# Performance work log

Hardware: AMD Instinct MI355X
Metric: run time of the kernel (lower is better)

The kernel has to match this reference:

```python
import jax, jax.numpy as jnp
import numpy as np

H = 150
PASSES = 5
NSETS = 2
N = 50000
E = 400000
G = 64
SLOPE = 0.01  # torch leaky_relu default


def setup_inputs() -> dict:
    key = jax.random.key(0)
    ks = jax.random.split(key, 20)
    def u(k, shape, fan):
        lim = 1.0 / np.sqrt(fan)
        return jax.random.uniform(k, shape, jnp.float32, -lim, lim)
    return {
        "nodes": jax.random.normal(ks[0], (N, H), jnp.float32),
        "problem_type": jax.random.uniform(ks[1], (G, 1), jnp.float32),
        "edge_W": u(ks[2], (NSETS, H, H), H),
        "edge_b": u(ks[3], (NSETS, H), H),
        "gru_w_ih": u(ks[4], (3 * H, H), H),
        "gru_w_hh": u(ks[5], (3 * H, H), H),
        "gru_b_ih": u(ks[6], (3 * H,), H),
        "gru_b_hh": u(ks[7], (3 * H,), H),
        "fc1_w": u(ks[8], (80, 151), 151),
        "fc1_b": u(ks[9], (80,), 151),
        "fc2_w": u(ks[10], (80, 80), 80),
        "fc2_b": u(ks[11], (80,), 80),
        "fcL_w": u(ks[12], (10, 80), 80),
        "fcL_b": u(ks[13], (10,), 80),
        "edges": jax.random.randint(ks[14], (NSETS, E, 2), 0, N),
        "graph_ids": jnp.sort(jax.random.randint(ks[15], (N,), 0, G)),
        "tbptt": 0,
    }


def _gru_cell(x, h, w_ih, w_hh, b_ih, b_hh):
    gi = x @ w_ih.T + b_ih  # [N, 3H]
    gh = h @ w_hh.T + b_hh
    ir, iz, inn = jnp.split(gi, 3, axis=-1)
    hr, hz, hn = jnp.split(gh, 3, axis=-1)
    r = jax.nn.sigmoid(ir + hr)
    z = jax.nn.sigmoid(iz + hz)
    n = jnp.tanh(inn + r * hn)
    return (1.0 - z) * n + z * h


def reference(nodes, problem_type, edge_W, edge_b, gru_w_ih, gru_w_hh,
              gru_b_ih, gru_b_hh, fc1_w, fc1_b, fc2_w, fc2_b, fcL_w, fcL_b,
              edges, graph_ids, tbptt):
    n_sets = edge_W.shape[0]
    n_graphs = problem_type.shape[0]
    for j in range(PASSES):
        incoming = jnp.zeros_like(nodes)
        for k in range(n_sets):
            src = edges[k, :, 1]
            dst = edges[k, :, 0]
            # NOTE: in the source, the first Linear+leaky_relu result is
            # overwritten; the effective edge message is just the second Linear.
            y = nodes[src] @ edge_W[k].T + edge_b[k]  # [E, H]
            incoming = incoming.at[dst].add(y)
        nodes = _gru_cell(incoming, nodes, gru_w_ih, gru_w_hh, gru_b_ih, gru_b_hh)
        if tbptt == 1 and j < PASSES - 2:
            nodes = jax.lax.stop_gradient(nodes)
    g = jax.ops.segment_sum(nodes, graph_ids, num_segments=n_graphs)  # [G, H]
    g = jnp.log(g)
    g = jnp.where(jnp.isnan(g), 0.0, g)
    g = jax.nn.relu(g)
    x = jnp.concatenate([g, problem_type], axis=1)  # [G, 151]
    x = jax.nn.leaky_relu(x @ fc1_w.T + fc1_b, SLOPE)
    x = jax.nn.leaky_relu(x @ fc2_w.T + fc2_b, SLOPE)
    return x @ fcL_w.T + fcL_b  # [G, 10]
```

## Files before the change

kernel.cpp:

```cpp
#include <hip/hip_runtime.h>
#include <stdint.h>

#define NN 50000
#define H 150
#define NE 400000
#define NG 64
#define NPASS 5
#define KB 480
#define VC 640
#define NRB 391

typedef unsigned short u16;
typedef unsigned int u32;
typedef __attribute__((ext_vector_type(8))) short short8;
typedef __attribute__((ext_vector_type(4))) float float4v;
typedef __attribute__((ext_vector_type(4))) u32 uint4v;

__device__ __forceinline__ u16 f2bf_rn(float x) {
  union { float f; u32 u; } v; v.f = x;
  u32 r = v.u + 0x7fffu + ((v.u >> 16) & 1u);
  return (u16)(r >> 16);
}
__device__ __forceinline__ float bf2f(u16 h) {
  union { u32 u; float f; } v; v.u = ((u32)h) << 16;
  return v.f;
}
__device__ __forceinline__ u32 packf(float v) {
  u16 hi = f2bf_rn(v);
  u16 lo = f2bf_rn(v - bf2f(hi));
  return (u32)hi | ((u32)lo << 16);
}
__device__ __forceinline__ float upk(u32 u) {
  union { u32 u; float f; } a, b;
  a.u = u << 16; b.u = u & 0xffff0000u;
  return a.f + b.f;
}
__device__ __forceinline__ void async16(const void* g, void* l) {
  __builtin_amdgcn_global_load_lds(
      (const __attribute__((address_space(1))) unsigned int*)(uintptr_t)g,
      (__attribute__((address_space(3))) unsigned int*)(uint32_t)(uintptr_t)l,
      16, 0, 0);
}

__global__ void hist_kernel(const int* __restrict__ edges, int* __restrict__ cnt) {
  int id = blockIdx.x * 256 + threadIdx.x;
  if (id >= 2 * NE) return;
  int dst = edges[id * 2];
  int set = id / NE;
  atomicAdd(&cnt[dst * 2 + set], 1);
}

__global__ __launch_bounds__(1024) void scan1_kernel(const int* __restrict__ cnt,
                                                     int* __restrict__ rowptr,
                                                     int* __restrict__ bsum, int n) {
  __shared__ int sd[1024];
  int t = threadIdx.x;
  int idx = blockIdx.x * 1024 + t;
  int v = (idx < n) ? cnt[idx] : 0;
  sd[t] = v;
  __syncthreads();
  for (int off = 1; off < 1024; off <<= 1) {
    int add = (t >= off) ? sd[t - off] : 0;
    __syncthreads();
    sd[t] += add;
    __syncthreads();
  }
  if (idx < n) rowptr[idx] = sd[t] - v;
  if (t == 1023) bsum[blockIdx.x] = sd[1023];
}

__global__ __launch_bounds__(128) void scan2_kernel(const int* __restrict__ bsum,
                                                    int* __restrict__ boff, int nb) {
  __shared__ int sd[128];
  int t = threadIdx.x;
  int v = (t < nb) ? bsum[t] : 0;
  sd[t] = v;
  __syncthreads();
  for (int off = 1; off < 128; off <<= 1) {
    int add = (t >= off) ? sd[t - off] : 0;
    __syncthreads();
    sd[t] += add;
    __syncthreads();
  }
  boff[t] = sd[t] - v;
}

__global__ void scan3_kernel(int* __restrict__ rowptr, const int* __restrict__ boff, int n) {
  int idx = blockIdx.x * 256 + threadIdx.x;
  if (idx < n) rowptr[idx] += boff[idx >> 10];
}

__global__ void total_kernel(int* __restrict__ rowptr, const int* __restrict__ boff, int n, int nb) {
  if (threadIdx.x == 0 && blockIdx.x == 0) rowptr[n] = boff[nb];
}

__global__ void copy_int_kernel(const int* __restrict__ a, int* __restrict__ b, int n) {
  int id = blockIdx.x * 256 + threadIdx.x;
  if (id < n) b[id] = a[id];
}

__global__ void fill_kernel(const int* __restrict__ edges, int* __restrict__ cursor,
                            u16* __restrict__ colbuf) {
  int id = blockIdx.x * 256 + threadIdx.x;
  if (id >= 2 * NE) return;
  int dst = edges[id * 2];
  int src = edges[id * 2 + 1];
  int set = id / NE;
  int pos = atomicAdd(&cursor[dst * 2 + set], 1);
  colbuf[pos] = (u16)src;
}

__global__ void bounds_kernel(const int* __restrict__ gids, int* __restrict__ gstart) {
  int g = threadIdx.x;
  if (g > NG) return;
  int lo = 0, hi = NN;
  while (lo < hi) { int m = (lo + hi) >> 1; if (gids[m] < g) lo = m + 1; else hi = m; }
  gstart[g] = lo;
}

__global__ void build_B_kernel(const float* __restrict__ wih, const float* __restrict__ whh,
                               const float* __restrict__ eW,
                               u16* __restrict__ Bh, u16* __restrict__ Bl) {
  int id = blockIdx.x * 256 + threadIdx.x;
  if (id >= VC * KB) return;
  int v = id / KB, k = id % KB;
  int g = (v >> 4) & 3, c = (v >> 6) * 16 + (v & 15);
  int seg = k / 160, kk = k % 160;
  float val = 0.f;
  if (c < H && kk < H) {
    if (seg < 2) {
      if (g < 3) {
        const float* wr = wih + (size_t)(g * H + c) * H;
        const float* wc = eW + (size_t)seg * H * H + kk;
        float acc = 0.f;
        for (int t = 0; t < H; t++) acc += wr[t] * wc[(size_t)t * H];
        val = acc;
      }
    } else {
      if (g == 0) val = whh[(size_t)c * H + kk];
      else if (g == 1) val = whh[(size_t)(H + c) * H + kk];
      else if (g == 3) val = whh[(size_t)(2 * H + c) * H + kk];
    }
  }
  u16 h = f2bf_rn(val);
  Bh[id] = h;
  Bl[id] = f2bf_rn(val - bf2f(h));
}

__global__ void build_coef_kernel(const float* __restrict__ wih,
                                  const float* __restrict__ eb,
                                  const float* __restrict__ bih, const float* __restrict__ bhh,
                                  float* __restrict__ coefs) {
  int id = threadIdx.x + blockIdx.x * 256;
  if (id >= VC) return;
  int g = id / 160, c = id % 160;
  float u0 = 0.f, u1 = 0.f, bs = 0.f;
  if (c < H) {
    if (g < 3) {
      const float* wr = wih + (size_t)(g * H + c) * H;
      for (int t = 0; t < H; t++) { u0 += wr[t] * eb[t]; u1 += wr[t] * eb[H + t]; }
    }
    if (g == 0) bs = bih[c] + bhh[c];
    else if (g == 1) bs = bih[H + c] + bhh[H + c];
    else if (g == 2) bs = bih[2 * H + c];
    else bs = bhh[2 * H + c];
  }
  coefs[id] = u0;
  coefs[VC + id] = u1;
  coefs[2 * VC + id] = bs;
}

__global__ void init_nodes_kernel(const float* __restrict__ nin,
                                  u32* __restrict__ npkA, u32* __restrict__ npkB) {
  int id = blockIdx.x * 256 + threadIdx.x;
  if (id >= NN * 160) return;
  int r = id / 160, c = id % 160;
  if (c < H) {
    npkA[id] = packf(nin[(size_t)r * H + c]);
  } else {
    npkA[id] = 0;
    npkB[id] = 0;
  }
}

__global__ void pad_S_kernel(u32* __restrict__ Snp) {
  int id = blockIdx.x * 256 + threadIdx.x;
  if (id >= NN * 20) return;
  int r = id / 20, rem = id % 20;
  int set = rem / 10, t = rem % 10;
  Snp[(size_t)r * 320 + set * 160 + H + t] = 0;
}

__global__ __launch_bounds__(256) void gather_kernel(
    const u32* __restrict__ npk, const int* __restrict__ rowptr,
    const u16* __restrict__ colbuf, u32* __restrict__ Snp) {
  int gtid = blockIdx.x * 256 + threadIdx.x;
  int wid = gtid >> 6;
  if (wid >= 2 * NN) return;
  int node = wid >> 1, set = wid & 1;
  int lane = gtid & 63;
  int s = rowptr[2 * node + set], e = rowptr[2 * node + set + 1];
  int deg = e - s;
  int c4 = 4 * lane;
  bool ok = (lane < 40);
  float a0 = 0.f, a1 = 0.f, a2 = 0.f, a3 = 0.f;
  for (int base = 0; base < deg; base += 64) {
    int rem = min(64, deg - base);
    u32 srcv = 0;
    if (lane < rem) srcv = (u32)colbuf[s + base + lane];
    int i = 0;
    for (; i + 3 < rem; i += 4) {
      int r0 = __builtin_amdgcn_readlane((int)srcv, i);
      int r1 = __builtin_amdgcn_readlane((int)srcv, i + 1);
      int r2 = __builtin_amdgcn_readlane((int)srcv, i + 2);
      int r3 = __builtin_amdgcn_readlane((int)srcv, i + 3);
      uint4v v0 = {0, 0, 0, 0}, v1 = {0, 0, 0, 0};
      uint4v v2 = {0, 0, 0, 0}, v3 = {0, 0, 0, 0};
      if (ok) {
        v0 = *(const uint4v*)(npk + (size_t)(u32)r0 * 160 + c4);
        v1 = *(const uint4v*)(npk + (size_t)(u32)r1 * 160 + c4);
        v2 = *(const uint4v*)(npk + (size_t)(u32)r2 * 160 + c4);
        v3 = *(const uint4v*)(npk + (size_t)(u32)r3 * 160 + c4);
      }
      a0 += upk(v0.x) + upk(v1.x);
      a1 += upk(v0.y) + upk(v1.y);
      a2 += upk(v0.z) + upk(v1.z);
      a3 += upk(v0.w) + upk(v1.w);
      a0 += upk(v2.x) + upk(v3.x);
      a1 += upk(v2.y) + upk(v3.y);
      a2 += upk(v2.z) + upk(v3.z);
      a3 += upk(v2.w) + upk(v3.w);
    }
    for (; i + 1 < rem; i += 2) {
      int r0 = __builtin_amdgcn_readlane((int)srcv, i);
      int r1 = __builtin_amdgcn_readlane((int)srcv, i + 1);
      uint4v v0 = {0, 0, 0, 0}, v1 = {0, 0, 0, 0};
      if (ok) {
        v0 = *(const uint4v*)(npk + (size_t)(u32)r0 * 160 + c4);
        v1 = *(const uint4v*)(npk + (size_t)(u32)r1 * 160 + c4);
      }
      a0 += upk(v0.x) + upk(v1.x);
      a1 += upk(v0.y) + upk(v1.y);
      a2 += upk(v0.z) + upk(v1.z);
      a3 += upk(v0.w) + upk(v1.w);
    }
    if (i < rem) {
      int r0 = __builtin_amdgcn_readlane((int)srcv, i);
      uint4v v0 = {0, 0, 0, 0};
      if (ok) v0 = *(const uint4v*)(npk + (size_t)(u32)r0 * 160 + c4);
      a0 += upk(v0.x);
      a1 += upk(v0.y);
      a2 += upk(v0.z);
      a3 += upk(v0.w);
    }
  }
  if (ok) {
    uint4v pv;
    pv.x = packf(a0);
    pv.y = packf(a1);
    pv.z = packf(a2);
    pv.w = packf(a3);
    *(uint4v*)(Snp + (size_t)node * 320 + set * 160 + c4) = pv;
  }
}


template<int KT>
__device__ __forceinline__ void stage_fn(
    const u32* __restrict__ Snp, const u32* __restrict__ npkc,
    const u16* __restrict__ Bhp, const u16* __restrict__ Blp,
    char* Ab, char* Bb, int tid, int w, int r0, int ccb) {
  #pragma unroll
  for (int i = 0; i < 4; i++) {
    int cl = i * 256 + tid;
    int row = cl >> 3;
    int q = (cl & 7) ^ (row & 7);
    int rg = min(r0 + row, NN - 1);
    if constexpr (KT < 10)
      async16(Snp + (size_t)rg * 320 + KT * 32 + q * 4, Ab + i * 4096 + w * 1024);
    else
      async16(npkc + (size_t)rg * 160 + (KT - 10) * 32 + q * 4, Ab + i * 4096 + w * 1024);
  }
  constexpr int koffB = (KT < 10) ? KT * 32 : 320 + (KT - 10) * 32;
  constexpr int skipg = (KT < 10) ? 3 : 2;
  #pragma unroll
  for (int i = 0; i < 2; i++) {
    int cl = i * 256 + tid;
    int row = cl >> 2;
    int q = (cl & 3) ^ ((row >> 1) & 3);
    if (((row >> 4) & 3) != skipg) {
      size_t gb = (size_t)(ccb * 128 + row) * KB + koffB + q * 8;
      int lb = i * 4096 + w * 1024;
      async16(Bhp + gb, Bb + lb);
      async16(Blp + gb, Bb + 8192 + lb);
    }
  }
}

template<int KTn>
__device__ __forceinline__ void read_frags_fn(
    const char* Ab, const char* Bb, int m, int quad, int mrow0, int nco0,
    uint4v (&A0)[4], uint4v (&A1)[4], short8 (&RBh)[3], short8 (&RBl)[3]) {
  #pragma unroll
  for (int jj = 0; jj < 3; jj++) {
    const int jsel = (jj == 2) ? ((KTn < 10) ? 2 : 3) : jj;
    int br = nco0 + jsel * 16 + m;
    int bd = br * 64 + ((quad ^ ((br >> 1) & 3)) * 16);
    RBh[jj] = *(const short8*)(Bb + bd);
    RBl[jj] = *(const short8*)(Bb + 8192 + bd);
  }
  #pragma unroll
  for (int mt = 0; mt < 4; mt++) {
    int r = mrow0 + mt * 16 + m;
    A0[mt] = *(const uint4v*)(Ab + r * 128 + (((2 * quad) ^ (r & 7)) * 16));
    A1[mt] = *(const uint4v*)(Ab + r * 128 + (((2 * quad + 1) ^ (r & 7)) * 16));
  }
}

template<int KT>
__device__ __forceinline__ void mfma_fn(
    const uint4v (&A0)[4], const uint4v (&A1)[4],
    const short8 (&MBh)[3], const short8 (&MBl)[3], float4v (&acc)[4][4]) {
  #pragma unroll
  for (int mt = 0; mt < 4; mt++) {
    u32 uu[8] = {A0[mt].x, A0[mt].y, A0[mt].z, A0[mt].w,
                 A1[mt].x, A1[mt].y, A1[mt].z, A1[mt].w};
    short8 ah, al;
    #pragma unroll
    for (int e2 = 0; e2 < 8; e2++) {
      ah[e2] = (short)(uu[e2] & 0xffffu);
      al[e2] = (short)(uu[e2] >> 16);
    }
    #pragma unroll
    for (int jj = 0; jj < 3; jj++) {
      const int J = (KT < 10) ? jj : ((jj == 2) ? 3 : jj);
      acc[mt][J] = __builtin_amdgcn_mfma_f32_16x16x32_bf16(ah, MBh[jj], acc[mt][J], 0, 0, 0);
      acc[mt][J] = __builtin_amdgcn_mfma_f32_16x16x32_bf16(ah, MBl[jj], acc[mt][J], 0, 0, 0);
      acc[mt][J] = __builtin_amdgcn_mfma_f32_16x16x32_bf16(al, MBh[jj], acc[mt][J], 0, 0, 0);
    }
  }
}

template<int KT>
__device__ __forceinline__ void gemm_step(
    const u32* __restrict__ Snp, const u32* __restrict__ npkc,
    const u16* __restrict__ Bhp, const u16* __restrict__ Blp,
    char (&Abuf)[16384], char (&Bbuf)[16384],
    int tid, int w, int m, int quad, int mrow0, int nco0, int r0, int ccb,
    float4v (&acc)[4][4]) {
  uint4v A0[4], A1[4];
  short8 FBh[3], FBl[3];
  read_frags_fn<KT>(Abuf, Bbuf, m, quad, mrow0, nco0, A0, A1, FBh, FBl);
  asm volatile("s_waitcnt lgkmcnt(0)" ::: "memory");
  __builtin_amdgcn_sched_barrier(0);
  __builtin_amdgcn_s_barrier();
  if constexpr (KT + 1 <= 14)
    stage_fn<KT + 1>(Snp, npkc, Bhp, Blp, Abuf, Bbuf, tid, w, r0, ccb);
  __builtin_amdgcn_sched_barrier(0);
  __builtin_amdgcn_s_setprio(1);
  mfma_fn<KT>(A0, A1, FBh, FBl, acc);
  __builtin_amdgcn_s_setprio(0);
  __builtin_amdgcn_sched_barrier(0);
  if constexpr (KT + 1 <= 14) {
    asm volatile("s_waitcnt vmcnt(0)" ::: "memory");
    __builtin_amdgcn_sched_barrier(0);
    __builtin_amdgcn_s_barrier();
  }
}

__global__ __launch_bounds__(256, 4) void gru_gemm_kernel(
    const u32* __restrict__ Snp, const u32* __restrict__ npkc,
    const u16* __restrict__ Bhp, const u16* __restrict__ Blp,
    const float* __restrict__ coefs, const int* __restrict__ rowptr,
    u32* __restrict__ npkn) {
  __shared__ char Abuf[16384];
  __shared__ char Bbuf[16384];
  const int bid = blockIdx.x;
  const int xcd = bid & 7;
  const int rest = bid >> 3;
  const int ccb = rest % 5;
  const int r0b = (rest / 5) * 8 + xcd;
  if (r0b >= NRB) return;
  const int r0 = r0b * 128;
  const int tid = threadIdx.x;
  const int w = tid >> 6, l = tid & 63;
  const int m = l & 15, quad = l >> 4;
  const int mrow0 = (w & 1) * 64;
  const int nco0 = (w >> 1) * 64;

  float4v acc[4][4];
  #pragma unroll
  for (int mt = 0; mt < 4; mt++)
    #pragma unroll
    for (int j = 0; j < 4; j++) acc[mt][j] = (float4v){0.f, 0.f, 0.f, 0.f};

  stage_fn<0>(Snp, npkc, Bhp, Blp, Abuf, Bbuf, tid, w, r0, ccb);
  asm volatile("s_waitcnt vmcnt(0)" ::: "memory");
  __builtin_amdgcn_sched_barrier(0);
  __builtin_amdgcn_s_barrier();

  #define STEP(K) gemm_step<K>(Snp, npkc, Bhp, Blp, Abuf, Bbuf, tid, w, m, quad, \
                               mrow0, nco0, r0, ccb, acc)
  STEP(0);  STEP(1);  STEP(2);  STEP(3);  STEP(4);
  STEP(5);  STEP(6);  STEP(7);  STEP(8);  STEP(9);
  STEP(10); STEP(11); STEP(12); STEP(13); STEP(14);
  #undef STEP

  int c = (ccb * 2 + (w >> 1)) * 16 + m;
  if (c >= H) return;
  float u0r = coefs[c],            u0z = coefs[160 + c],
        u0n = coefs[320 + c];
  float u1r = coefs[VC + c],       u1z = coefs[VC + 160 + c],
        u1n = coefs[VC + 320 + c];
  float bsr = coefs[2 * VC + c],   bsz = coefs[2 * VC + 160 + c],
        bsn = coefs[2 * VC + 320 + c], bsh = coefs[2 * VC + 480 + c];
  #pragma unroll
  for (int mt = 0; mt < 4; mt++) {
    #pragma unroll
    for (int i = 0; i < 4; i++) {
      int row = r0 + mrow0 + mt * 16 + quad * 4 + i;
      if (row >= NN) continue;
      float d0 = (float)(rowptr[2 * row + 1] - rowptr[2 * row]);
      float d1 = (float)(rowptr[2 * row + 2] - rowptr[2 * row + 1]);
      float pr = acc[mt][0][i] + d0 * u0r + d1 * u1r + bsr;
      float pz = acc[mt][1][i] + d0 * u0z + d1 * u1z + bsz;
      float pn = acc[mt][2][i] + d0 * u0n + d1 * u1n + bsn;
      float ph = acc[mt][3][i] + bsh;
      float r_g = 1.f / (1.f + __expf(-pr));
      float z_g = 1.f / (1.f + __expf(-pz));
      float narg = pn + r_g * ph;
      float e2 = __expf(2.f * narg);
      float n_g = 1.f - 2.f / (e2 + 1.f);
      float h = upk(npkc[(size_t)row * 160 + c]);
      npkn[(size_t)row * 160 + c] = packf((1.f - z_g) * n_g + z_g * h);
    }
  }
}

__global__ __launch_bounds__(192) void segsum_kernel(const u32* __restrict__ npk,
                                                     const int* __restrict__ gstart,
                                                     float* __restrict__ gsum) {
  int g = blockIdx.x, chunk = blockIdx.y;
  int c = threadIdx.x;
  if (c >= H) return;
  int s = gstart[g], e = gstart[g + 1];
  int len = e - s;
  if (len <= 0) return;
  int per = (len + 3) / 4;
  int rs = s + chunk * per;
  int re = min(e, rs + per);
  if (rs >= re) return;
  float acc = 0.f;
  for (int r = rs; r < re; r++) acc += upk(npk[(size_t)r * 160 + c]);
  atomicAdd(&gsum[g * H + c], acc);
}

__global__ __launch_bounds__(192) void head_kernel(
    const float* __restrict__ gsum, const float* __restrict__ pt,
    const float* __restrict__ fc1_w, const float* __restrict__ fc1_b,
    const float* __restrict__ fc2_w, const float* __restrict__ fc2_b,
    const float* __restrict__ fcL_w, const float* __restrict__ fcL_b,
    float* __restrict__ out) {
  __shared__ float x[151];
  __shared__ float x1[80];
  __shared__ float x2[80];
  int row = blockIdx.x;
  int t = threadIdx.x;
  if (t < 151) {
    float v;
    if (t < H) { float g = gsum[row * H + t]; v = (g > 1.f) ? logf(g) : 0.f; }
    else v = pt[row];
    x[t] = v;
  }
  __syncthreads();
  if (t < 80) {
    float acc = fc1_b[t];
    const float* wrow = fc1_w + t * 151;
    #pragma unroll 4
    for (int k = 0; k < 151; k++) acc += x[k] * wrow[k];
    x1[t] = (acc > 0.f) ? acc : 0.01f * acc;
  }
  __syncthreads();
  if (t < 80) {
    float acc = fc2_b[t];
    const float* wrow = fc2_w + t * 80;
    #pragma unroll 4
    for (int k = 0; k < 80; k++) acc += x1[k] * wrow[k];
    x2[t] = (acc > 0.f) ? acc : 0.01f * acc;
  }
  __syncthreads();
  if (t < 10) {
    float acc = fcL_b[t];
    const float* wrow = fcL_w + t * 80;
    #pragma unroll 4
    for (int k = 0; k < 80; k++) acc += x2[k] * wrow[k];
    out[row * 10 + t] = acc;
  }
}

extern "C" void kernel_launch(void* const* d_in, const int* in_sizes, int n_in,
                              void* d_out, int out_size, void* d_ws, size_t ws_size,
                              hipStream_t stream) {
  const float* nodes_in = (const float*)d_in[0];
  const float* problem_type = (const float*)d_in[1];
  const float* edge_W = (const float*)d_in[2];
  const float* edge_b = (const float*)d_in[3];
  const float* w_ih = (const float*)d_in[4];
  const float* w_hh = (const float*)d_in[5];
  const float* b_ih = (const float*)d_in[6];
  const float* b_hh = (const float*)d_in[7];
  const float* fc1_w = (const float*)d_in[8];
  const float* fc1_b = (const float*)d_in[9];
  const float* fc2_w = (const float*)d_in[10];
  const float* fc2_b = (const float*)d_in[11];
  const float* fcL_w = (const float*)d_in[12];
  const float* fcL_b = (const float*)d_in[13];
  const int* edges = (const int*)d_in[14];
  const int* graph_ids = (const int*)d_in[15];

  char* ws = (char*)d_ws;
  size_t off = 0;
  auto alloc = [&](size_t bytes) -> void* {
    void* p = ws + off;
    off = (off + bytes + 255) & ~(size_t)255;
    return p;
  };
  u32* npkA     = (u32*)alloc((size_t)NN * 160 * 4);
  u32* npkB     = (u32*)alloc((size_t)NN * 160 * 4);
  u32* Snp      = (u32*)alloc((size_t)NN * 320 * 4);
  u16* Bh       = (u16*)alloc((size_t)VC * KB * 2);
  u16* Bl       = (u16*)alloc((size_t)VC * KB * 2);
  float* coefs  = (float*)alloc(3 * VC * 4);
  int* rowptr   = (int*)alloc((2 * NN + 1) * 4);
  int* cursor   = (int*)alloc(2 * NN * 4);
  u16* colbuf   = (u16*)alloc(2ull * NE * 2);
  int* bsum     = (int*)alloc(128 * 4);
  int* boff     = (int*)alloc(128 * 4);
  int* gstart   = (int*)alloc((NG + 1) * 4);
  float* gsum   = (float*)alloc((size_t)NG * H * 4);

  const int n2 = 2 * NN;
  const int nb = (n2 + 1023) / 1024;

  hipMemsetAsync(cursor, 0, n2 * 4, stream);
  hist_kernel<<<(2 * NE + 255) / 256, 256, 0, stream>>>(edges, cursor);
  scan1_kernel<<<nb, 1024, 0, stream>>>(cursor, rowptr, bsum, n2);
  scan2_kernel<<<1, 128, 0, stream>>>(bsum, boff, nb);
  scan3_kernel<<<(n2 + 255) / 256, 256, 0, stream>>>(rowptr, boff, n2);
  total_kernel<<<1, 64, 0, stream>>>(rowptr, boff, n2, nb);
  copy_int_kernel<<<(n2 + 255) / 256, 256, 0, stream>>>(rowptr, cursor, n2);
  fill_kernel<<<(2 * NE + 255) / 256, 256, 0, stream>>>(edges, cursor, colbuf);
  bounds_kernel<<<1, 128, 0, stream>>>(graph_ids, gstart);
  build_B_kernel<<<(VC * KB + 255) / 256, 256, 0, stream>>>(w_ih, w_hh, edge_W, Bh, Bl);
  build_coef_kernel<<<(VC + 255) / 256, 256, 0, stream>>>(w_ih, edge_b, b_ih, b_hh, coefs);
  init_nodes_kernel<<<(NN * 160 + 255) / 256, 256, 0, stream>>>(nodes_in, npkA, npkB);
  pad_S_kernel<<<(NN * 20 + 255) / 256, 256, 0, stream>>>(Snp);

  const int ngrp = (NRB + 7) / 8;
  u32* nbuf[2] = {npkA, npkB};
  for (int pass = 0; pass < NPASS; pass++) {
    u32* cur = nbuf[pass & 1];
    u32* nxt = nbuf[1 - (pass & 1)];
    gather_kernel<<<(2 * NN * 64 + 255) / 256, 256, 0, stream>>>(cur, rowptr, colbuf, Snp);
    gru_gemm_kernel<<<ngrp * 5 * 8, 256, 0, stream>>>(
        Snp, cur, Bh, Bl, coefs, rowptr, nxt);
  }
  u32* fin = nbuf[NPASS & 1];

  hipMemsetAsync(gsum, 0, (size_t)NG * H * 4, stream);
  segsum_kernel<<<dim3(NG, 4), 192, 0, stream>>>(fin, gstart, gsum);
  head_kernel<<<NG, 192, 0, stream>>>(gsum, problem_type, fc1_w, fc1_b, fc2_w, fc2_b,
                                      fcL_w, fcL_b, (float*)d_out);
}
```

Before: 1.128 ms.

## Process two K-tiles per barrier step with double-buffered LDS staging

Restructures the GRU GEMM main loop so each superstep reads fragments for two K-tiles from two LDS buffers, stages the next two tiles, then issues both tiles' MFMAs. This halves the number of barrier/waitcnt synchronisation points and gives longer MFMA runs to hide global loads. In exchange, LDS per block doubles to 64KB and register pressure grows, so the launch bound drops from 4 to 2 blocks per CU and occupancy falls.

```diff
diff --git a/kernel.cpp b/kernel.cpp
--- a/kernel.cpp
+++ b/kernel.cpp
@@ -341,40 +341,48 @@
   }
 }
 
-template<int KT>
-__device__ __forceinline__ void gemm_step(
+template<int K0>
+__device__ __forceinline__ void gemm_superstep(
     const u32* __restrict__ Snp, const u32* __restrict__ npkc,
     const u16* __restrict__ Bhp, const u16* __restrict__ Blp,
-    char (&Abuf)[16384], char (&Bbuf)[16384],
+    char (&Abuf)[2][16384], char (&Bbuf)[2][16384],
     int tid, int w, int m, int quad, int mrow0, int nco0, int r0, int ccb,
     float4v (&acc)[4][4]) {
-  uint4v A0[4], A1[4];
-  short8 FBh[3], FBl[3];
-  read_frags_fn<KT>(Abuf, Bbuf, m, quad, mrow0, nco0, A0, A1, FBh, FBl);
+  constexpr int K1 = K0 + 1;
+  uint4v A0a[4], A1a[4], A0b[4], A1b[4];
+  short8 FBha[3], FBla[3], FBhb[3], FBlb[3];
+  read_frags_fn<K0>(Abuf[0], Bbuf[0], m, quad, mrow0, nco0, A0a, A1a, FBha, FBla);
+  if constexpr (K1 <= 14)
+    read_frags_fn<K1>(Abuf[1], Bbuf[1], m, quad, mrow0, nco0, A0b, A1b, FBhb, FBlb);
   asm volatile("s_waitcnt lgkmcnt(0)" ::: "memory");
   __builtin_amdgcn_sched_barrier(0);
-  __builtin_amdgcn_s_barrier();
-  if constexpr (KT + 1 <= 14)
-    stage_fn<KT + 1>(Snp, npkc, Bhp, Blp, Abuf, Bbuf, tid, w, r0, ccb);
-  __builtin_amdgcn_sched_barrier(0);
+  if constexpr (K0 + 2 <= 14) {
+    __builtin_amdgcn_s_barrier();
+    stage_fn<K0 + 2>(Snp, npkc, Bhp, Blp, Abuf[0], Bbuf[0], tid, w, r0, ccb);
+    if constexpr (K1 + 2 <= 14)
+      stage_fn<K1 + 2>(Snp, npkc, Bhp, Blp, Abuf[1], Bbuf[1], tid, w, r0, ccb);
+    __builtin_amdgcn_sched_barrier(0);
+  }
   __builtin_amdgcn_s_setprio(1);
-  mfma_fn<KT>(A0, A1, FBh, FBl, acc);
+  mfma_fn<K0>(A0a, A1a, FBha, FBla, acc);
+  if constexpr (K1 <= 14)
+    mfma_fn<K1>(A0b, A1b, FBhb, FBlb, acc);
   __builtin_amdgcn_s_setprio(0);
   __builtin_amdgcn_sched_barrier(0);
-  if constexpr (KT + 1 <= 14) {
+  if constexpr (K0 + 2 <= 14) {
     asm volatile("s_waitcnt vmcnt(0)" ::: "memory");
     __builtin_amdgcn_sched_barrier(0);
     __builtin_amdgcn_s_barrier();
   }
 }
 
-__global__ __launch_bounds__(256, 4) void gru_gemm_kernel(
+__global__ __launch_bounds__(256, 2) void gru_gemm_kernel(
     const u32* __restrict__ Snp, const u32* __restrict__ npkc,
     const u16* __restrict__ Bhp, const u16* __restrict__ Blp,
     const float* __restrict__ coefs, const int* __restrict__ rowptr,
     u32* __restrict__ npkn) {
-  __shared__ char Abuf[16384];
-  __shared__ char Bbuf[16384];
+  __shared__ char Abuf[2][16384];
+  __shared__ char Bbuf[2][16384];
   const int bid = blockIdx.x;
   const int xcd = bid & 7;
   const int rest = bid >> 3;
@@ -394,17 +402,17 @@
     #pragma unroll
     for (int j = 0; j < 4; j++) acc[mt][j] = (float4v){0.f, 0.f, 0.f, 0.f};
 
-  stage_fn<0>(Snp, npkc, Bhp, Blp, Abuf, Bbuf, tid, w, r0, ccb);
+  stage_fn<0>(Snp, npkc, Bhp, Blp, Abuf[0], Bbuf[0], tid, w, r0, ccb);
+  stage_fn<1>(Snp, npkc, Bhp, Blp, Abuf[1], Bbuf[1], tid, w, r0, ccb);
   asm volatile("s_waitcnt vmcnt(0)" ::: "memory");
   __builtin_amdgcn_sched_barrier(0);
   __builtin_amdgcn_s_barrier();
 
-  #define STEP(K) gemm_step<K>(Snp, npkc, Bhp, Blp, Abuf, Bbuf, tid, w, m, quad, \
-                               mrow0, nco0, r0, ccb, acc)
-  STEP(0);  STEP(1);  STEP(2);  STEP(3);  STEP(4);
-  STEP(5);  STEP(6);  STEP(7);  STEP(8);  STEP(9);
-  STEP(10); STEP(11); STEP(12); STEP(13); STEP(14);
-  #undef STEP
+  #define SSTEP(K) gemm_superstep<K>(Snp, npkc, Bhp, Blp, Abuf, Bbuf, tid, w, m, \
+                                     quad, mrow0, nco0, r0, ccb, acc)
+  SSTEP(0); SSTEP(2); SSTEP(4); SSTEP(6);
+  SSTEP(8); SSTEP(10); SSTEP(12); SSTEP(14);
+  #undef SSTEP
 
   int c = (ccb * 2 + (w >> 1)) * 16 + m;
   if (c >= H) return;
```

New measurement: 1.110 ms. Within noise of the previous version (-1.6%).
